# Kernel optimization log

Hardware: AMD Instinct MI355X
Metric: run time of the kernel (lower is better)

The kernel has to match this reference:

```python
import math
import jax, jax.numpy as jnp
import numpy as np

HEADS = 8
DIM_HEAD = 64
NUM_MEM_KV = 16


def alibi_slopes(heads):
    def pow2_slopes(n):
        start = 2 ** (-(2 ** -(math.log2(n) - 3)))
        return [start * (start ** i) for i in range(n)]
    if math.log2(heads).is_integer():
        return np.asarray(pow2_slopes(heads), dtype=np.float32)
    cp2 = 2 ** math.floor(math.log2(heads))
    extra = pow2_slopes(2 * cp2)[0::2][: heads - cp2]
    return np.asarray(pow2_slopes(cp2) + extra, dtype=np.float32)


def setup_inputs() -> dict:
    key = jax.random.key(0)
    ks = jax.random.split(key, 12)
    b, n, dim = 2, 2048, 512
    h, dh, mem = HEADS, DIM_HEAD, NUM_MEM_KV
    s = 0.02  # weight init scale for numerical sanity
    return {
        "x": jax.random.normal(ks[0], (b, n, dim), jnp.float32),
        "Wq": jax.random.normal(ks[1], (dim, h * dh), jnp.float32) * s,
        "Wk": jax.random.normal(ks[2], (dim, h * dh), jnp.float32) * s,
        "Wv": jax.random.normal(ks[3], (dim, h * dh), jnp.float32) * s,
        "mem_k": jax.random.normal(ks[4], (h, mem, dh), jnp.float32),
        "mem_v": jax.random.normal(ks[5], (h, mem, dh), jnp.float32),
        "pre_proj": jax.random.normal(ks[6], (h, h), jnp.float32),
        "post_proj": jax.random.normal(ks[7], (h, h), jnp.float32),
        "head_scale_params": jnp.ones((1, h, 1, 1), jnp.float32),
        "Wout": jax.random.normal(ks[8], (h * dh, dim), jnp.float32) * s,
        "bout": jnp.zeros((dim,), jnp.float32),
    }


def reference(x, Wq, Wk, Wv, mem_k, mem_v, pre_proj, post_proj,
              head_scale_params, Wout, bout):
    b, n, dim = x.shape
    h, dh, mem = HEADS, DIM_HEAD, NUM_MEM_KV
    scale = dh ** -0.5

    def split_heads(t):  # [b,n,h*dh] -> [b,h,n,dh]
        return t.reshape(b, n, h, dh).transpose(0, 2, 1, 3)

    q = split_heads(x @ Wq)
    k = split_heads(x @ Wk)
    v = split_heads(x @ Wv)

    # prepend learned memory key/values: k,v -> [b,h,mem+n,dh]
    k = jnp.concatenate([jnp.broadcast_to(mem_k, (b, h, mem, dh)), k], axis=2)
    v = jnp.concatenate([jnp.broadcast_to(mem_v, (b, h, mem, dh)), v], axis=2)
    j = mem + n

    dots = jnp.einsum('bhid,bhjd->bhij', q, k) * scale
    # talking heads (pre-softmax)
    dots = jnp.einsum('bhij,hk->bkij', dots, pre_proj)
    # alibi relative positional bias: arange(j) * slope per head
    slopes = jnp.asarray(alibi_slopes(h))  # [h]
    dots = dots + jnp.arange(j, dtype=dots.dtype)[None, None, None, :] * slopes[None, :, None, None]
    # causal mask (mem columns always visible); mask where col-mem > row
    neg = -jnp.finfo(dots.dtype).max
    causal = (jnp.arange(j)[None, :] - mem) > jnp.arange(n)[:, None]  # [n,j]
    dots = jnp.where(causal[None, None], neg, dots)

    attn = jax.nn.softmax(dots, axis=-1)
    # talking heads (post-softmax)
    attn = jnp.einsum('bhij,hk->bkij', attn, post_proj)

    out = jnp.einsum('bhij,bhjd->bhid', attn, v)
    out = out * head_scale_params
    out = out.transpose(0, 2, 1, 3).reshape(b, n, h * dh)
    return out @ Wout + bout
```

## Files before the change

kernel.cpp:

```cpp
#include <hip/hip_runtime.h>
#include <math.h>

namespace {
constexpr int B = 2;
constexpr int N = 2048;
constexpr int DIM = 512;
constexpr int H = 8;
constexpr int MEM = 16;
constexpr int J = MEM + N;
constexpr int CHUNK = 512;
constexpr int CMAXS = 5;
constexpr float S2 = 0.125f * 1.4426950408889634f;
constexpr size_t EPB = 17170432;
}

typedef __attribute__((ext_vector_type(8))) short short8;
typedef __attribute__((ext_vector_type(2))) float floatx2;
typedef __attribute__((ext_vector_type(4))) float floatx4;
typedef __attribute__((ext_vector_type(4))) unsigned short ushortx4;
typedef __attribute__((ext_vector_type(8))) unsigned short ushortx8;
typedef __attribute__((ext_vector_type(4))) unsigned int uintx4;

__device__ inline unsigned short f2bf(float f) {
    unsigned int u = __float_as_uint(f);
    u += 0x7fffu + ((u >> 16) & 1u);
    return (unsigned short)(u >> 16);
}
__device__ inline unsigned int pk2bf(float a, float b) {
    return ((__float_as_uint(a) + 0x8000u) >> 16) |
           ((__float_as_uint(b) + 0x8000u) & 0xffff0000u);
}

__global__ __launch_bounds__(256)
void x_conv(const float* __restrict__ x, unsigned short* __restrict__ x16)
{
    const size_t base = ((size_t)blockIdx.x * 256 + threadIdx.x) * 8;
    const float4 a = *(const float4*)(x + base);
    const float4 b = *(const float4*)(x + base + 4);
    ushortx8 o = { f2bf(a.x), f2bf(a.y), f2bf(a.z), f2bf(a.w),
                   f2bf(b.x), f2bf(b.y), f2bf(b.z), f2bf(b.w) };
    *(ushortx8*)(x16 + base) = o;
}

__global__ __launch_bounds__(256)
void wt_conv(const float* __restrict__ Wq, const float* __restrict__ Wk,
             const float* __restrict__ Wv, const float* __restrict__ Wo,
             unsigned short* __restrict__ tq, unsigned short* __restrict__ tk,
             unsigned short* __restrict__ tv, unsigned short* __restrict__ to_)
{
    const int z = blockIdx.z;
    const float* __restrict__ W = (z == 0) ? Wq : (z == 1) ? Wk : (z == 2) ? Wv : Wo;
    unsigned short* __restrict__ WT = (z == 0) ? tq : (z == 1) ? tk : (z == 2) ? tv : to_;
    const int k0 = blockIdx.x * 64, n0 = blockIdx.y * 64;

    __shared__ __align__(16) unsigned short tile[64][72];
    const int t = threadIdx.x;
    const int rrow = t >> 4, rcol = (t & 15) * 4;
#pragma unroll
    for (int rr = 0; rr < 4; ++rr) {
        const int row = rrow + rr * 16;
        const float4 v = *(const float4*)(W + (size_t)(k0 + row) * DIM + n0 + rcol);
        tile[rcol + 0][row] = f2bf(v.x);
        tile[rcol + 1][row] = f2bf(v.y);
        tile[rcol + 2][row] = f2bf(v.z);
        tile[rcol + 3][row] = f2bf(v.w);
    }
    __syncthreads();
    const int orow = t >> 2, oseg = (t & 3) * 16;
    *(ushortx8*)(WT + (size_t)(n0 + orow) * DIM + k0 + oseg) =
        *(const ushortx8*)(&tile[orow][oseg]);
    *(ushortx8*)(WT + (size_t)(n0 + orow) * DIM + k0 + oseg + 8) =
        *(const ushortx8*)(&tile[orow][oseg + 8]);
}

__global__ __launch_bounds__(256)
void qkv_gemm(const unsigned short* __restrict__ x16, const unsigned short* __restrict__ tq,
              const unsigned short* __restrict__ tk, const unsigned short* __restrict__ tv,
              unsigned short* __restrict__ q16, unsigned short* __restrict__ kcat,
              unsigned short* __restrict__ vt16)
{
    const int which = blockIdx.z;
    const unsigned short* __restrict__ WT = (which == 0) ? tq : (which == 1) ? tk : tv;
    const int t = threadIdx.x;
    const int lane = t & 63, w = t >> 6;
    const int iL = lane & 15, quad = lane >> 4;
    const int mb = blockIdx.x * 64;
    const int n0 = blockIdx.y * 64;

    __shared__ __align__(16) unsigned short As[2][64][32];
    __shared__ __align__(16) unsigned short Bs[2][64][32];

    const int r0 = t >> 2, s8 = (t & 3) * 8;

    floatx4 acc[4];
#pragma unroll
    for (int ng = 0; ng < 4; ++ng) acc[ng] = (floatx4){0.f, 0.f, 0.f, 0.f};

    {
        *(ushortx8*)(&As[0][r0][s8]) =
            *(const ushortx8*)(x16 + (size_t)(mb + r0) * DIM + s8);
        *(ushortx8*)(&Bs[0][r0][s8]) =
            *(const ushortx8*)(WT + (size_t)(n0 + r0) * DIM + s8);
    }
    __syncthreads();

#pragma unroll
    for (int it = 0; it < 16; ++it) {
        const int buf = it & 1;
        if (it + 1 < 16) {
            const int k0 = (it + 1) * 32;
            const ushortx8 av = *(const ushortx8*)(x16 + (size_t)(mb + r0) * DIM + k0 + s8);
            const ushortx8 bv = *(const ushortx8*)(WT + (size_t)(n0 + r0) * DIM + k0 + s8);
            *(ushortx8*)(&As[buf ^ 1][r0][s8]) = av;
            *(ushortx8*)(&Bs[buf ^ 1][r0][s8]) = bv;
        }
        const short8 af = *(const short8*)(&As[buf][w * 16 + iL][quad * 8]);
#pragma unroll
        for (int ng = 0; ng < 4; ++ng) {
            const short8 bf = *(const short8*)(&Bs[buf][ng * 16 + iL][quad * 8]);
            acc[ng] = __builtin_amdgcn_mfma_f32_16x16x32_bf16(af, bf, acc[ng], 0, 0, 0);
        }
        __syncthreads();
    }

    const int mbw = mb + w * 16;
    const int h0 = n0 >> 6;
    if (which == 2) {
#pragma unroll
        for (int ng = 0; ng < 4; ++ng) {
            const int d = ng * 16 + iL;
#pragma unroll
            for (int r = 0; r < 4; ++r) {
                const int m = mbw + quad * 4 + r;
                const int bb = m >> 11, ii = m & (N - 1);
                vt16[((size_t)(bb * H + h0) * 64 + d) * J + MEM + ii] = f2bf(acc[ng][r]);
            }
        }
    } else if (which == 1) {
#pragma unroll
        for (int ng = 0; ng < 4; ++ng) {
            const int d = ng * 16 + iL;
#pragma unroll
            for (int r = 0; r < 4; ++r) {
                const int m = mbw + quad * 4 + r;
                const int bb = m >> 11, ii = m & (N - 1);
                kcat[((size_t)bb * J + MEM + ii) * 512 + h0 * 64 + d] = f2bf(acc[ng][r]);
            }
        }
    } else {
#pragma unroll
        for (int ng = 0; ng < 4; ++ng) {
            const int d = ng * 16 + iL;
#pragma unroll
            for (int r = 0; r < 4; ++r) {
                const int m = mbw + quad * 4 + r;
                const int bb = m >> 11, ii = m & (N - 1);
                q16[((size_t)(bb * H + h0) * N + ii) * 64 + d] = f2bf(acc[ng][r]);
            }
        }
    }
}

__global__ void memkv_copy(const float* __restrict__ mem_k, const float* __restrict__ mem_v,
                           unsigned short* __restrict__ kcat, unsigned short* __restrict__ vt16)
{
    const int idx = blockIdx.x * 256 + threadIdx.x;
    if (idx >= H * MEM * 64) return;
    const int h0 = idx >> 10;
    const int rd = idx & 1023;
    const int r = rd >> 6, d = rd & 63;
    const unsigned short kk = f2bf(mem_k[idx]);
    const unsigned short vv = f2bf(mem_v[idx]);
#pragma unroll
    for (int bb = 0; bb < B; ++bb) {
        kcat[((size_t)bb * J + r) * 512 + h0 * 64 + d] = kk;
        vt16[((size_t)(bb * H + h0) * 64 + d) * J + r] = vv;
    }
}

__global__ __launch_bounds__(256)
void attn_scores(const unsigned short* __restrict__ qb, const unsigned short* __restrict__ kc,
                 const float* __restrict__ prep, float* __restrict__ lbuf,
                 unsigned short* __restrict__ e16)
{
    const int tt = blockIdx.x, c = 4 - blockIdx.y, b = blockIdx.z;
    const int i0 = tt * 16;
    const int jlim = i0 + 32;
    const int jstart = c * CHUNK;
    if (jstart >= jlim) return;
    const int jend = min(jstart + CHUNK, jlim);
    const int nwin = (jend - jstart) >> 4;

    __shared__ __align__(16) unsigned short k_s[2][16][512];

    const int t = threadIdx.x;
    const int lane = t & 63, w = t >> 6;
    const int iL = lane & 15, quad = lane >> 4;
    const int i = i0 + iL;

    const size_t krowbase = (size_t)b * J * 512;

    auto STAGE = [&](int buf, int jw0) {
#pragma unroll
        for (int rr = 0; rr < 4; ++rr) {
            const int row = rr * 4 + w;
            const int j = jw0 + row;
            const char* src = (const char*)(kc + krowbase + (size_t)j * 512);
            const int soff = (lane * 16) ^ ((j & 7) << 4);
            __builtin_amdgcn_global_load_lds(
                (const __attribute__((address_space(1))) unsigned int*)(src + soff),
                (__attribute__((address_space(3))) unsigned int*)(&k_s[buf][row][0]),
                16, 0, 0);
        }
    };

    STAGE(0, jstart);

    const int h1a = 2 * w, h1b = 2 * w + 1;
    short8 qfA[16], qfB[16];
#pragma unroll
    for (int ks = 0; ks < 16; ++ks) {
        const int h0 = ks >> 1;
        const float sA = prep[h0 * 8 + h1a];
        const float sB = prep[h0 * 8 + h1b];
        const ushortx8 raw = *(const ushortx8*)(
            qb + ((size_t)(b * H + h0) * N + i0 + iL) * 64 + (ks & 1) * 32 + quad * 8);
        uintx4 ua, ub;
#pragma unroll
        for (int e2 = 0; e2 < 4; ++e2) {
            const float f0 = __uint_as_float((unsigned int)raw[e2 * 2] << 16);
            const float f1 = __uint_as_float((unsigned int)raw[e2 * 2 + 1] << 16);
            ua[e2] = pk2bf(f0 * sA, f1 * sA);
            ub[e2] = pk2bf(f0 * sB, f1 * sB);
        }
        qfA[ks] = __builtin_bit_cast(short8, ua);
        qfB[ks] = __builtin_bit_cast(short8, ub);
    }
    __syncthreads();

    const float slA = 1.4426950408889634f / (float)(2 << h1a);
    const float slB = 1.4426950408889634f / (float)(2 << h1b);
    const size_t ebase = (size_t)b * EPB + (size_t)(8 * tt * tt + 24 * tt) * 128;
    float l0 = 0.f, l1 = 0.f;

    for (int n = 0; n < nwin; ++n) {
        const int buf = n & 1;
        if (n + 1 < nwin) STAGE(buf ^ 1, jstart + (n + 1) * 16);
        const int jw0 = jstart + n * 16;

        floatx4 a0 = {0.f, 0.f, 0.f, 0.f}, a1 = {0.f, 0.f, 0.f, 0.f};
#pragma unroll
        for (int ks = 0; ks < 16; ++ks) {
            const int off = (ks * 32 + quad * 8) ^ ((iL & 7) << 3);
            const short8 aF = *(const short8*)(&k_s[buf][iL][off]);
            a0 = __builtin_amdgcn_mfma_f32_16x16x32_bf16(aF, qfA[ks], a0, 0, 0, 0);
            a1 = __builtin_amdgcn_mfma_f32_16x16x32_bf16(aF, qfB[ks], a1, 0, 0, 0);
        }

#pragma unroll
        for (int r = 0; r < 4; ++r) {
            const int j = jw0 + quad * 4 + r;
            const int jm = j - MEM;
            const bool vis = jm <= i;
            const float bias = (float)(jm - i);
            const float e0 = vis ? exp2f(fmaf(a0[r], S2, slA * bias)) : 0.f;
            const float e1 = vis ? exp2f(fmaf(a1[r], S2, slB * bias)) : 0.f;
            l0 += e0; l1 += e1;
            *(unsigned int*)(e16 + ebase + ((size_t)j * 16 + iL) * 8 + h1a) = pk2bf(e0, e1);
        }
        __syncthreads();
    }

    l0 += __shfl_xor(l0, 16); l0 += __shfl_xor(l0, 32);
    l1 += __shfl_xor(l1, 16); l1 += __shfl_xor(l1, 32);
    if (quad == 0) {
        atomicAdd(lbuf + ((size_t)(b * 128 + tt) * 8 + h1a) * 16 + iL, l0);
        atomicAdd(lbuf + ((size_t)(b * 128 + tt) * 8 + h1b) * 16 + iL, l1);
    }
}

__global__ __launch_bounds__(256)
void attn_pv2(const unsigned short* __restrict__ e16, const unsigned short* __restrict__ vt,
              const float* __restrict__ postp, const float* __restrict__ hsp,
              const float* __restrict__ lbuf, float* __restrict__ ao)
{
    const int tt = blockIdx.x, c = 4 - blockIdx.y, b = blockIdx.z;
    const int i0 = tt * 16;
    const int jlim = i0 + 32;
    const int jstart = c * CHUNK;
    if (jstart >= jlim) return;
    const int jend = min(jstart + CHUNK, jlim);
    const int nw = (jend - jstart + 31) >> 5;

    __shared__ __align__(16) unsigned short p2s[2][8][16][40];
    __shared__ __align__(16) float post_s[64];

    const int t = threadIdx.x;
    if (t < 64) post_s[t] = postp[t] * hsp[t & 7];

    const int lane = t & 63, w = t >> 6;
    const int iL = lane & 15, quad = lane >> 4;
    const int dW = w * 16 + iL;
    const int i_p = t & 15;
    const int jj = t >> 4;
    const size_t ebase = (size_t)b * EPB + (size_t)(8 * tt * tt + 24 * tt) * 128;
    const unsigned short* __restrict__ ep = e16 + ebase + (size_t)i_p * 8;

    float linv[8];
#pragma unroll
    for (int h1 = 0; h1 < 8; ++h1)
        linv[h1] = 1.0f / lbuf[((size_t)(b * 128 + tt) * 8 + h1) * 16 + i_p];

    floatx4 y[8];
#pragma unroll
    for (int h2 = 0; h2 < 8; ++h2) y[h2] = (floatx4){0.f, 0.f, 0.f, 0.f};

    ushortx8 evA[2], evB[2], evC[2];
    {
        const int j0c = jstart + jj * 2;
        int ja = min(j0c, jend - 1), jb2 = min(j0c + 1, jend - 1);
        evA[0] = *(const ushortx8*)(ep + (size_t)(ja * 16) * 8);
        evA[1] = *(const ushortx8*)(ep + (size_t)(jb2 * 16) * 8);
        ja = min(j0c + 32, jend - 1); jb2 = min(j0c + 33, jend - 1);
        evB[0] = *(const ushortx8*)(ep + (size_t)(ja * 16) * 8);
        evB[1] = *(const ushortx8*)(ep + (size_t)(jb2 * 16) * 8);
        ja = min(j0c + 64, jend - 1); jb2 = min(j0c + 65, jend - 1);
        evC[0] = *(const ushortx8*)(ep + (size_t)(ja * 16) * 8);
        evC[1] = *(const ushortx8*)(ep + (size_t)(jb2 * 16) * 8);
    }
    __syncthreads();

    for (int n = 0; n < nw; ++n) {
        const int jw0 = jstart + n * 32;
        const int buf = n & 1;

        int jbv = jw0 + quad * 8;
        if (jbv > J - 8) jbv = J - 8;
        short8 bF[8];
#pragma unroll
        for (int h2 = 0; h2 < 8; ++h2)
            bF[h2] = *(const short8*)(vt + ((size_t)(b * H + h2) * 64 + dW) * J + jbv);

        ushortx8 evT0, evT1;
        {
            const int wn = (n + 3 < nw) ? n + 3 : nw - 1;
            const int j0n = jstart + wn * 32 + jj * 2;
            const int ja = min(j0n, jend - 1), jb2 = min(j0n + 1, jend - 1);
            evT0 = *(const ushortx8*)(ep + (size_t)(ja * 16) * 8);
            evT1 = *(const ushortx8*)(ep + (size_t)(jb2 * 16) * 8);
        }

        floatx2 p2v[2][4];
#pragma unroll
        for (int s = 0; s < 2; ++s) {
#pragma unroll
            for (int q = 0; q < 4; ++q) p2v[s][q] = (floatx2){0.f, 0.f};
            const int j = jw0 + jj * 2 + s;
            if (j < jend) {
#pragma unroll
                for (int h1 = 0; h1 < 8; ++h1) {
                    const float e = __uint_as_float(
                        (unsigned int)(unsigned short)evA[s][h1] << 16) * linv[h1];
                    const floatx2* po = (const floatx2*)(&post_s[h1 * 8]);
                    p2v[s][0] += e * po[0];
                    p2v[s][1] += e * po[1];
                    p2v[s][2] += e * po[2];
                    p2v[s][3] += e * po[3];
                }
            }
        }
#pragma unroll
        for (int h2 = 0; h2 < 8; ++h2)
            *(unsigned int*)(&p2s[buf][h2][i_p][jj * 2]) =
                pk2bf(p2v[0][h2 >> 1][h2 & 1], p2v[1][h2 >> 1][h2 & 1]);
        __syncthreads();

#pragma unroll
        for (int h2 = 0; h2 < 8; ++h2) {
            const short8 aF = *(const short8*)(&p2s[buf][h2][iL][quad * 8]);
            y[h2] = __builtin_amdgcn_mfma_f32_16x16x32_bf16(aF, bF[h2], y[h2], 0, 0, 0);
        }
        evA[0] = evB[0]; evA[1] = evB[1];
        evB[0] = evC[0]; evB[1] = evC[1];
        evC[0] = evT0;   evC[1] = evT1;
    }

#pragma unroll
    for (int h2 = 0; h2 < 8; ++h2) {
#pragma unroll
        for (int r = 0; r < 4; ++r) {
            const int ii = i0 + quad * 4 + r;
            atomicAdd(ao + ((size_t)b * N + ii) * DIM + h2 * 64 + dW, y[h2][r]);
        }
    }
}

__global__ __launch_bounds__(256)
void out_gemm(const float* __restrict__ ain, const unsigned short* __restrict__ WT,
              const float* __restrict__ bo, float* __restrict__ out)
{
    const int t = threadIdx.x;
    const int lane = t & 63, w = t >> 6;
    const int iL = lane & 15, quad = lane >> 4;
    const int mb = blockIdx.x * 64;
    const int n0 = blockIdx.y * 64;

    __shared__ __align__(16) unsigned short As[2][64][32];
    __shared__ __align__(16) unsigned short Bs[2][64][32];

    const int ar0 = t >> 3, as4 = (t & 7) * 4;
    const int br0 = t >> 2, bs8 = (t & 3) * 8;

    floatx4 acc[4];
#pragma unroll
    for (int ng = 0; ng < 4; ++ng) acc[ng] = (floatx4){0.f, 0.f, 0.f, 0.f};

    {
        const float4 v0 = *(const float4*)(ain + (size_t)(mb + ar0) * DIM + as4);
        const float4 v1 = *(const float4*)(ain + (size_t)(mb + ar0 + 32) * DIM + as4);
        ushortx4 o0 = { f2bf(v0.x), f2bf(v0.y), f2bf(v0.z), f2bf(v0.w) };
        ushortx4 o1 = { f2bf(v1.x), f2bf(v1.y), f2bf(v1.z), f2bf(v1.w) };
        *(ushortx4*)(&As[0][ar0][as4]) = o0;
        *(ushortx4*)(&As[0][ar0 + 32][as4]) = o1;
        *(ushortx8*)(&Bs[0][br0][bs8]) =
            *(const ushortx8*)(WT + (size_t)(n0 + br0) * DIM + bs8);
    }
    __syncthreads();

#pragma unroll
    for (int it = 0; it < 16; ++it) {
        const int buf = it & 1;
        if (it + 1 < 16) {
            const int k0 = (it + 1) * 32;
            const float4 v0 = *(const float4*)(ain + (size_t)(mb + ar0) * DIM + k0 + as4);
            const float4 v1 = *(const float4*)(ain + (size_t)(mb + ar0 + 32) * DIM + k0 + as4);
            const ushortx8 bv =
                *(const ushortx8*)(WT + (size_t)(n0 + br0) * DIM + k0 + bs8);
            ushortx4 o0 = { f2bf(v0.x), f2bf(v0.y), f2bf(v0.z), f2bf(v0.w) };
            ushortx4 o1 = { f2bf(v1.x), f2bf(v1.y), f2bf(v1.z), f2bf(v1.w) };
            *(ushortx4*)(&As[buf ^ 1][ar0][as4]) = o0;
            *(ushortx4*)(&As[buf ^ 1][ar0 + 32][as4]) = o1;
            *(ushortx8*)(&Bs[buf ^ 1][br0][bs8]) = bv;
        }
        const short8 af = *(const short8*)(&As[buf][w * 16 + iL][quad * 8]);
#pragma unroll
        for (int ng = 0; ng < 4; ++ng) {
            const short8 bf = *(const short8*)(&Bs[buf][ng * 16 + iL][quad * 8]);
            acc[ng] = __builtin_amdgcn_mfma_f32_16x16x32_bf16(af, bf, acc[ng], 0, 0, 0);
        }
        __syncthreads();
    }

    const int mbw = mb + w * 16;
#pragma unroll
    for (int ng = 0; ng < 4; ++ng) {
        const int n = n0 + ng * 16 + iL;
        const float bias = bo[n];
#pragma unroll
        for (int r = 0; r < 4; ++r) {
            const int m = mbw + quad * 4 + r;
            out[(size_t)m * DIM + n] = acc[ng][r] + bias;
        }
    }
}

extern "C" void kernel_launch(void* const* d_in, const int* in_sizes, int n_in,
                              void* d_out, int out_size, void* d_ws, size_t ws_size,
                              hipStream_t stream)
{
    (void)in_sizes; (void)n_in; (void)out_size; (void)ws_size;
    const float* x      = (const float*)d_in[0];
    const float* Wq     = (const float*)d_in[1];
    const float* Wk     = (const float*)d_in[2];
    const float* Wv     = (const float*)d_in[3];
    const float* mem_k  = (const float*)d_in[4];
    const float* mem_v  = (const float*)d_in[5];
    const float* pre_p  = (const float*)d_in[6];
    const float* post_p = (const float*)d_in[7];
    const float* hs     = (const float*)d_in[8];
    const float* Wo     = (const float*)d_in[9];
    const float* bo     = (const float*)d_in[10];
    float* out = (float*)d_out;

    constexpr size_t NAO  = (size_t)B * N * DIM;
    constexpr size_t NLB  = (size_t)B * 128 * H * 16;
    constexpr size_t NW   = (size_t)DIM * DIM;
    constexpr size_t NQ   = (size_t)B * H * N * 64;
    constexpr size_t NK   = (size_t)B * J * 512;
    constexpr size_t NX   = (size_t)B * N * DIM;

    float* ws = (float*)d_ws;
    float* ao   = ws;
    float* lbuf = ao + NAO;
    unsigned short* wtq  = (unsigned short*)(lbuf + NLB);
    unsigned short* wtk  = wtq + NW;
    unsigned short* wtv  = wtk + NW;
    unsigned short* wto  = wtv + NW;
    unsigned short* q16  = wto + NW;
    unsigned short* kcat = q16 + NQ;
    unsigned short* v16  = kcat + NK;
    unsigned short* x16  = v16 + NK;
    unsigned short* e16  = x16 + NX;

    x_conv<<<dim3(1024), 256, 0, stream>>>(x, x16);
    wt_conv<<<dim3(8, 8, 4), 256, 0, stream>>>(Wq, Wk, Wv, Wo, wtq, wtk, wtv, wto);
    qkv_gemm<<<dim3(64, 8, 3), 256, 0, stream>>>(x16, wtq, wtk, wtv, q16, kcat, v16);
    memkv_copy<<<dim3(32), 256, 0, stream>>>(mem_k, mem_v, kcat, v16);
    hipMemsetAsync(ao, 0, (NAO + NLB) * sizeof(float), stream);
    attn_scores<<<dim3(128, CMAXS, B), 256, 0, stream>>>(q16, kcat, pre_p, lbuf, e16);
    attn_pv2<<<dim3(128, CMAXS, B), 256, 0, stream>>>(e16, v16, post_p, hs, lbuf, ao);
    out_gemm<<<dim3(64, 8), 256, 0, stream>>>(ao, wto, bo, out);
}
```

Measured before the change: 253.1 us.

## Split attention score work one head per wave with 512-thread blocks

```diff
diff --git a/kernel.cpp b/kernel.cpp
--- a/kernel.cpp
+++ b/kernel.cpp
@@ -178,7 +178,7 @@
     }
 }
 
-__global__ __launch_bounds__(256)
+__global__ __launch_bounds__(512, 4)
 void attn_scores(const unsigned short* __restrict__ qb, const unsigned short* __restrict__ kc,
                  const float* __restrict__ prep, float* __restrict__ lbuf,
                  unsigned short* __restrict__ e16)
@@ -191,7 +191,7 @@
     const int jend = min(jstart + CHUNK, jlim);
     const int nwin = (jend - jstart) >> 4;
 
-    __shared__ __align__(16) unsigned short k_s[2][16][512];
+    __shared__ __align__(16) unsigned short k_s[2][16][520];
 
     const int t = threadIdx.x;
     const int lane = t & 63, w = t >> 6;
@@ -202,13 +202,12 @@
 
     auto STAGE = [&](int buf, int jw0) {
 #pragma unroll
-        for (int rr = 0; rr < 4; ++rr) {
-            const int row = rr * 4 + w;
+        for (int rr = 0; rr < 2; ++rr) {
+            const int row = rr * 8 + w;
             const int j = jw0 + row;
             const char* src = (const char*)(kc + krowbase + (size_t)j * 512);
-            const int soff = (lane * 16) ^ ((j & 7) << 4);
             __builtin_amdgcn_global_load_lds(
-                (const __attribute__((address_space(1))) unsigned int*)(src + soff),
+                (const __attribute__((address_space(1))) unsigned int*)(src + lane * 16),
                 (__attribute__((address_space(3))) unsigned int*)(&k_s[buf][row][0]),
                 16, 0, 0);
         }
@@ -216,67 +215,61 @@
 
     STAGE(0, jstart);
 
-    const int h1a = 2 * w, h1b = 2 * w + 1;
-    short8 qfA[16], qfB[16];
+    float pr[8];
+#pragma unroll
+    for (int h0 = 0; h0 < 8; ++h0) pr[h0] = prep[h0 * 8 + w];
+    short8 qf[16];
 #pragma unroll
     for (int ks = 0; ks < 16; ++ks) {
-        const int h0 = ks >> 1;
-        const float sA = prep[h0 * 8 + h1a];
-        const float sB = prep[h0 * 8 + h1b];
         const ushortx8 raw = *(const ushortx8*)(
-            qb + ((size_t)(b * H + h0) * N + i0 + iL) * 64 + (ks & 1) * 32 + quad * 8);
-        uintx4 ua, ub;
+            qb + ((size_t)(b * H + (ks >> 1)) * N + i0 + iL) * 64 + (ks & 1) * 32 + quad * 8);
+        const float s = pr[ks >> 1];
+        uintx4 u;
 #pragma unroll
         for (int e2 = 0; e2 < 4; ++e2) {
-            const float f0 = __uint_as_float((unsigned int)raw[e2 * 2] << 16);
-            const float f1 = __uint_as_float((unsigned int)raw[e2 * 2 + 1] << 16);
-            ua[e2] = pk2bf(f0 * sA, f1 * sA);
-            ub[e2] = pk2bf(f0 * sB, f1 * sB);
-        }
-        qfA[ks] = __builtin_bit_cast(short8, ua);
-        qfB[ks] = __builtin_bit_cast(short8, ub);
+            const float f0 = __uint_as_float((unsigned int)raw[e2 * 2] << 16) * s;
+            const float f1 = __uint_as_float((unsigned int)raw[e2 * 2 + 1] << 16) * s;
+            u[e2] = pk2bf(f0, f1);
+        }
+        qf[ks] = __builtin_bit_cast(short8, u);
     }
     __syncthreads();
 
-    const float slA = 1.4426950408889634f / (float)(2 << h1a);
-    const float slB = 1.4426950408889634f / (float)(2 << h1b);
+    const float sl = 1.4426950408889634f / (float)(2 << w);
     const size_t ebase = (size_t)b * EPB + (size_t)(8 * tt * tt + 24 * tt) * 128;
-    float l0 = 0.f, l1 = 0.f;
+    float l_acc = 0.f;
 
     for (int n = 0; n < nwin; ++n) {
         const int buf = n & 1;
         if (n + 1 < nwin) STAGE(buf ^ 1, jstart + (n + 1) * 16);
         const int jw0 = jstart + n * 16;
 
-        floatx4 a0 = {0.f, 0.f, 0.f, 0.f}, a1 = {0.f, 0.f, 0.f, 0.f};
-#pragma unroll
-        for (int ks = 0; ks < 16; ++ks) {
-            const int off = (ks * 32 + quad * 8) ^ ((iL & 7) << 3);
-            const short8 aF = *(const short8*)(&k_s[buf][iL][off]);
-            a0 = __builtin_amdgcn_mfma_f32_16x16x32_bf16(aF, qfA[ks], a0, 0, 0, 0);
-            a1 = __builtin_amdgcn_mfma_f32_16x16x32_bf16(aF, qfB[ks], a1, 0, 0, 0);
-        }
+        floatx4 aE = {0.f, 0.f, 0.f, 0.f}, aO = {0.f, 0.f, 0.f, 0.f};
+#pragma unroll
+        for (int ks = 0; ks < 16; ks += 2) {
+            const short8 f0 = *(const short8*)(&k_s[buf][iL][ks * 32 + quad * 8]);
+            const short8 f1 = *(const short8*)(&k_s[buf][iL][(ks + 1) * 32 + quad * 8]);
+            aE = __builtin_amdgcn_mfma_f32_16x16x32_bf16(f0, qf[ks], aE, 0, 0, 0);
+            aO = __builtin_amdgcn_mfma_f32_16x16x32_bf16(f1, qf[ks + 1], aO, 0, 0, 0);
+        }
+        const floatx4 a = aE + aO;
 
 #pragma unroll
         for (int r = 0; r < 4; ++r) {
             const int j = jw0 + quad * 4 + r;
             const int jm = j - MEM;
-            const bool vis = jm <= i;
-            const float bias = (float)(jm - i);
-            const float e0 = vis ? exp2f(fmaf(a0[r], S2, slA * bias)) : 0.f;
-            const float e1 = vis ? exp2f(fmaf(a1[r], S2, slB * bias)) : 0.f;
-            l0 += e0; l1 += e1;
-            *(unsigned int*)(e16 + ebase + ((size_t)j * 16 + iL) * 8 + h1a) = pk2bf(e0, e1);
+            const float e = (jm <= i)
+                ? exp2f(fmaf(a[r], S2, sl * (float)(jm - i))) : 0.f;
+            l_acc += e;
+            e16[ebase + ((size_t)j * 16 + iL) * 8 + w] = f2bf(e);
         }
         __syncthreads();
     }
 
-    l0 += __shfl_xor(l0, 16); l0 += __shfl_xor(l0, 32);
-    l1 += __shfl_xor(l1, 16); l1 += __shfl_xor(l1, 32);
-    if (quad == 0) {
-        atomicAdd(lbuf + ((size_t)(b * 128 + tt) * 8 + h1a) * 16 + iL, l0);
-        atomicAdd(lbuf + ((size_t)(b * 128 + tt) * 8 + h1b) * 16 + iL, l1);
-    }
+    l_acc += __shfl_xor(l_acc, 16);
+    l_acc += __shfl_xor(l_acc, 32);
+    if (quad == 0)
+        atomicAdd(lbuf + ((size_t)(b * 128 + tt) * 8 + w) * 16 + iL, l_acc);
 }
 
 __global__ __launch_bounds__(256)
@@ -507,7 +500,7 @@
     qkv_gemm<<<dim3(64, 8, 3), 256, 0, stream>>>(x16, wtq, wtk, wtv, q16, kcat, v16);
     memkv_copy<<<dim3(32), 256, 0, stream>>>(mem_k, mem_v, kcat, v16);
     hipMemsetAsync(ao, 0, (NAO + NLB) * sizeof(float), stream);
-    attn_scores<<<dim3(128, CMAXS, B), 256, 0, stream>>>(q16, kcat, pre_p, lbuf, e16);
+    attn_scores<<<dim3(128, CMAXS, B), 512, 0, stream>>>(q16, kcat, pre_p, lbuf, e16);
     attn_pv2<<<dim3(128, CMAXS, B), 256, 0, stream>>>(e16, v16, post_p, hs, lbuf, ao);
     out_gemm<<<dim3(64, 8), 256, 0, stream>>>(ao, wto, bo, out);
 }
```

New measurement: 266.6 us. 5.3% more time.
